# Optimization experiments

Hardware: AMD Instinct MI355X
Metric: run time of the kernel (lower is better)

Reference implementation:

```python
import jax, jax.numpy as jnp
import numpy as np

NUM_HEADS = 12
EMB = 768
D_KEY = 64
D_VALUE = 64
MASKED = True


def setup_inputs() -> dict:
    key = jax.random.key(0)
    k1, k2, k3, k4 = jax.random.split(key, 4)
    x = jax.random.normal(k1, (1, 4096, EMB), dtype=jnp.float32)
    q_proj = jax.random.normal(k2, (NUM_HEADS, EMB, D_KEY), dtype=jnp.float32)
    k_proj = jax.random.normal(k3, (NUM_HEADS, EMB, D_KEY), dtype=jnp.float32)
    v_proj = jax.random.normal(k4, (NUM_HEADS, EMB, D_VALUE), dtype=jnp.float32)
    return {"x": x, "q_proj": q_proj, "k_proj": k_proj, "v_proj": v_proj}


def reference(x, q_proj, k_proj, v_proj):
    # x: [B, S, E]; projections: [H, E, dk/dv]
    q = jnp.einsum("bse,hek->bhsk", x, q_proj)  # [B,H,S,dk]
    k = jnp.einsum("bse,hek->bhsk", x, k_proj)  # [B,H,S,dk]
    v = jnp.einsum("bse,hev->bhsv", x, v_proj)  # [B,H,S,dv]
    scale = jnp.sqrt(jnp.asarray(D_KEY, dtype=x.dtype))
    scores = jnp.einsum("bhsk,bhtk->bhst", q, k) / scale  # [B,H,S,S]
    if MASKED:
        S = x.shape[1]
        # causal mask: disallow attending to future positions (strict upper triangle)
        mask = jnp.triu(jnp.ones((S, S), dtype=bool), k=1)
        scores = jnp.where(mask, -jnp.inf, scores)
    attn = jax.nn.softmax(scores, axis=-1)
    out = jnp.einsum("bhst,bhtv->bhsv", attn, v)  # [B,H,S,dv]
    return out
```

## Files before the change

### kernel.cpp

```cpp
#include <hip/hip_runtime.h>
#include <hip/hip_bf16.h>

#define NH 12
#define SEQ 4096
#define E 768
#define DK 64

typedef float f32x4 __attribute__((ext_vector_type(4)));
typedef float f32x16 __attribute__((ext_vector_type(16)));
typedef __bf16 bf16x8 __attribute__((ext_vector_type(8)));
typedef __bf16 bf16x4 __attribute__((ext_vector_type(4)));
typedef unsigned u32x2 __attribute__((ext_vector_type(2)));
typedef unsigned u32x4 __attribute__((ext_vector_type(4)));

#define MFMA16(a, b, c) __builtin_amdgcn_mfma_f32_16x16x32_bf16((a), (b), (c), 0, 0, 0)
#define MFMA32(a, b, c) __builtin_amdgcn_mfma_f32_32x32x16_bf16((a), (b), (c), 0, 0, 0)

#define SCL 0.18033688011112042f
#define DEFER 10.8f

#define PART_SZ 4352

__device__ __forceinline__ void gload16(const void* g, void* l) {
    __builtin_amdgcn_global_load_lds(
        (const __attribute__((address_space(1))) void*)g,
        (__attribute__((address_space(3))) void*)l, 16, 0, 0);
}

__device__ __forceinline__ void block_sync() {
    __builtin_amdgcn_sched_barrier(0);
    __builtin_amdgcn_s_barrier();
    __builtin_amdgcn_sched_barrier(0);
}

__device__ __forceinline__ unsigned cvtpk(float lo, float hi) {
    unsigned r;
    asm("v_cvt_pk_bf16_f32 %0, %1, %2" : "=v"(r) : "v"(lo), "v"(hi));
    return r;
}
__device__ __forceinline__ u32x2 plswap(unsigned a, unsigned b) {
    return __builtin_amdgcn_permlane32_swap(a, b, false, false);
}
__device__ __forceinline__ float xhalf_max(float v) {
    u32x2 r = plswap(__float_as_uint(v), __float_as_uint(v));
    return fmaxf(__uint_as_float(r.x), __uint_as_float(r.y));
}
__device__ __forceinline__ float xhalf_add(float v) {
    u32x2 r = plswap(__float_as_uint(v), __float_as_uint(v));
    return __uint_as_float(r.x) + __uint_as_float(r.y);
}

__global__ __launch_bounds__(256) void prep_kernel(
    const float* __restrict__ x,
    const float* __restrict__ qp, const float* __restrict__ kp,
    const float* __restrict__ vp,
    __bf16* __restrict__ xh, __bf16* __restrict__ xl,
    __bf16* __restrict__ wtq_h, __bf16* __restrict__ wtq_l,
    __bf16* __restrict__ wtk_h, __bf16* __restrict__ wtk_l,
    __bf16* __restrict__ wtv_h) {
    __shared__ float tl[64][65];

    if (blockIdx.x >= 144) {
        int i = (blockIdx.x - 144) * 256 + threadIdx.x;
        float4 v = ((const float4*)x)[i];
        bf16x4 h, l;
        float vv[4] = {v.x, v.y, v.z, v.w};
#pragma unroll
        for (int j = 0; j < 4; ++j) {
            __bf16 hh = (__bf16)vv[j];
            h[j] = hh;
            l[j] = (__bf16)(vv[j] - (float)hh);
        }
        ((bf16x4*)xh)[i] = h;
        ((bf16x4*)xl)[i] = l;
        return;
    }

    const int h = blockIdx.x / 12;
    const int kt = blockIdx.x % 12;
    const int c = threadIdx.x & 63;
    const int r4 = threadIdx.x >> 6;

#pragma unroll
    for (int mat = 0; mat < 3; ++mat) {
        const float* src = ((mat == 0) ? qp : (mat == 1) ? kp : vp)
                         + (size_t)h * E * DK + (size_t)kt * 64 * DK;
        __syncthreads();
#pragma unroll
        for (int i = 0; i < 16; ++i) {
            int row = i * 4 + r4;
            tl[row][c] = src[row * DK + c];
        }
        __syncthreads();
#pragma unroll
        for (int i = 0; i < 16; ++i) {
            int n = i * 4 + r4;
            float v = tl[c][n];
            size_t o = (size_t)h * DK * E + (size_t)n * E + kt * 64 + c;
            if (mat == 0) {
                __bf16 hh = (__bf16)v;
                wtq_h[o] = hh;
                wtq_l[o] = (__bf16)(v - (float)hh);
            } else if (mat == 1) {
                float kk = v * SCL;
                __bf16 hh = (__bf16)kk;
                wtk_h[o] = hh;
                wtk_l[o] = (__bf16)(kk - (float)hh);
            } else {
                wtv_h[o] = (__bf16)v;
            }
        }
    }
}

__global__ __launch_bounds__(128, 2) void proj_kernel(
    const __bf16* __restrict__ xh, const __bf16* __restrict__ xl,
    const __bf16* __restrict__ wq_h_g, const __bf16* __restrict__ wq_l_g,
    const __bf16* __restrict__ wk_h_g, const __bf16* __restrict__ wk_l_g,
    const __bf16* __restrict__ wv_g,
    __bf16* __restrict__ qh_o, __bf16* __restrict__ ql_o,
    __bf16* __restrict__ kh_o, __bf16* __restrict__ kl_o,
    __bf16* __restrict__ vt_o) {
    __shared__ char wlds[2][20480];

    const int wg = (blockIdx.x & 7) * 96 + (blockIdx.x >> 3);
    const int head = wg >> 6;
    const int rb = wg & 63;
    const int wave = threadIdx.x >> 6;
    const int lane = threadIdx.x & 63;
    const int lrow = lane & 15;
    const int lk8 = (lane >> 4) * 8;
    const int g4 = (lane >> 4) * 4;
    const int rowbase = rb * 64 + wave * 32;

    const char* bases[5] = {
        (const char*)(wq_h_g + head * DK * E), (const char*)(wq_l_g + head * DK * E),
        (const char*)(wk_h_g + head * DK * E), (const char*)(wk_l_g + head * DK * E),
        (const char*)(wv_g + head * DK * E)};
    const int srow = lane >> 2;
    const int scol = (lane & 3) * 16;

    auto STAGE = [&](int buf, int ks) {
#pragma unroll
        for (int r = 0; r < 10; ++r) {
            int q = wave * 10 + r;
            const char* src = bases[q >> 2] + (size_t)((q & 3) * 16 + srow) * (E * 2) + ks * 64 + scol;
            gload16(src, wlds[buf] + q * 1024 + lane * 16);
        }
    };

    f32x4 accq[2][4], acck[2][4], accv[2][4];
#pragma unroll
    for (int rt = 0; rt < 2; ++rt)
#pragma unroll
        for (int f = 0; f < 4; ++f) {
            accq[rt][f] = (f32x4){0.f, 0.f, 0.f, 0.f};
            acck[rt][f] = (f32x4){0.f, 0.f, 0.f, 0.f};
            accv[rt][f] = (f32x4){0.f, 0.f, 0.f, 0.f};
        }

    bf16x8 ah[2], al[2], ahn[2], aln[2];
    auto LOADA = [&](int ks, bf16x8* h, bf16x8* l) {
#pragma unroll
        for (int rt = 0; rt < 2; ++rt) {
            size_t xo = (size_t)(rowbase + rt * 16 + lrow) * E + ks * 32 + lk8;
            h[rt] = *(const bf16x8*)(xh + xo);
            l[rt] = *(const bf16x8*)(xl + xo);
        }
    };

    LOADA(0, ah, al);
    STAGE(0, 0);
    int buf = 0;
    for (int ks = 0; ks < 24; ++ks) {
        if (ks < 23) {
            LOADA(ks + 1, ahn, aln);
            STAGE(buf ^ 1, ks + 1);
            asm volatile("s_waitcnt vmcnt(14)" ::: "memory");
        } else {
            asm volatile("s_waitcnt vmcnt(0)" ::: "memory");
        }
        block_sync();
#pragma unroll
        for (int f = 0; f < 4; ++f) {
            int bo = (f * 16 + lrow) * 64 + lk8 * 2;
            bf16x8 bqh = *(const bf16x8*)(wlds[buf] + bo);
            bf16x8 bql = *(const bf16x8*)(wlds[buf] + 4096 + bo);
            bf16x8 bkh = *(const bf16x8*)(wlds[buf] + 8192 + bo);
            bf16x8 bkl = *(const bf16x8*)(wlds[buf] + 12288 + bo);
            bf16x8 bv  = *(const bf16x8*)(wlds[buf] + 16384 + bo);
#pragma unroll
            for (int rt = 0; rt < 2; ++rt) {
                accq[rt][f] = MFMA16(ah[rt], bqh, accq[rt][f]);
                accq[rt][f] = MFMA16(ah[rt], bql, accq[rt][f]);
                accq[rt][f] = MFMA16(al[rt], bqh, accq[rt][f]);
                acck[rt][f] = MFMA16(ah[rt], bkh, acck[rt][f]);
                acck[rt][f] = MFMA16(ah[rt], bkl, acck[rt][f]);
                acck[rt][f] = MFMA16(al[rt], bkh, acck[rt][f]);
                accv[rt][f] = MFMA16(bv, ah[rt], accv[rt][f]);
            }
        }
        block_sync();
        if (ks < 23) {
#pragma unroll
            for (int rt = 0; rt < 2; ++rt) {
                ah[rt] = ahn[rt];
                al[rt] = aln[rt];
            }
        }
        buf ^= 1;
    }

    char* khb = (char*)kh_o + (size_t)head * SEQ * DK * 2;
    char* klb = (char*)kl_o + (size_t)head * SEQ * DK * 2;
    char* vb = (char*)vt_o + (size_t)head * DK * SEQ * 2;
#pragma unroll
    for (int rt = 0; rt < 2; ++rt)
#pragma unroll
        for (int f = 0; f < 4; ++f)
#pragma unroll
            for (int r = 0; r < 4; ++r) {
                int srow_o = rowbase + rt * 16 + g4 + r;
                int d = f * 16 + lrow;
                size_t o = (size_t)head * SEQ * DK + (size_t)srow_o * DK + d;
                float qv = accq[rt][f][r];
                __bf16 qhh = (__bf16)qv;
                qh_o[o] = qhh;
                ql_o[o] = (__bf16)(qv - (float)qhh);
                size_t ko = (size_t)(srow_o >> 6) * 8192 + ((srow_o >> 5) & 1) * 4096
                          + (size_t)f * 1024
                          + ((srow_o & 31) + 32 * ((lrow >> 3) & 1)) * 16 + (lrow & 7) * 2;
                float kv = acck[rt][f][r];
                __bf16 khh = (__bf16)kv;
                *(__bf16*)(khb + ko) = khh;
                *(__bf16*)(klb + ko) = (__bf16)(kv - (float)khh);
                int vd = f * 16 + g4 + r;
                int vs = rowbase + rt * 16 + lrow;
                size_t vo = (size_t)(vs >> 6) * 8192 + ((vd >> 5) & 1) * 4096
                          + ((vs >> 4) & 3) * 1024
                          + ((vd & 31) + 32 * ((vs >> 3) & 1)) * 16 + (vs & 7) * 2;
                *(__bf16*)(vb + vo) = (__bf16)accv[rt][f][r];
            }
}

__global__ __launch_bounds__(256, 2) void attn_part_kernel(
    const __bf16* __restrict__ qh, const __bf16* __restrict__ ql,
    const __bf16* __restrict__ kh, const __bf16* __restrict__ kl,
    const __bf16* __restrict__ vt,
    char* __restrict__ part) {
    const int blk = (blockIdx.x & 7) * 216 + (blockIdx.x >> 3);
    const int wave = threadIdx.x >> 6;
    const int task = blk * 4 + wave;
    const int lane = threadIdx.x & 63;
    const int lq = lane & 31;
    const int lh = lane >> 5;

    const int head = task / 576;
    const int t = task - head * 576;
    int g = 0;
#pragma unroll 8
    for (int gg = 1; gg <= 7; ++gg)
        if (t >= 16 * gg * (gg + 1) / 2) g = gg;
    const int nsp = g + 1;
    const int u = t - 16 * g * (g + 1) / 2;
    const int w = 16 * g + u / nsp;
    const int split = u - (u / nsp) * nsp;
    const int ktot = (w >> 1) + 1;
    const int lo = (split * ktot) / nsp;
    const int hi = ((split + 1) * ktot) / nsp;
    const int rowbase = w * 32;

    const size_t hoff = (size_t)head * SEQ * DK;

    bf16x8 qBh[4], qBl[4];
    {
        const __bf16* qph = qh + hoff + (size_t)(rowbase + lq) * DK + lh * 8;
        const __bf16* qpl = ql + hoff + (size_t)(rowbase + lq) * DK + lh * 8;
#pragma unroll
        for (int ds = 0; ds < 4; ++ds) {
            qBh[ds] = *(const bf16x8*)(qph + ds * 16);
            qBl[ds] = *(const bf16x8*)(qpl + ds * 16);
        }
    }

    const char* kh_p = (const char*)(kh + hoff) + (size_t)lo * 8192 + lane * 16;
    const char* kl_p = (const char*)(kl + hoff) + (size_t)lo * 8192 + lane * 16;
    const char* vt_p = (const char*)(vt + (size_t)head * DK * SEQ) + (size_t)lo * 8192 + lane * 16;

    f32x16 O0 = (f32x16)0.0f, O1 = (f32x16)0.0f;
    float m = -3.0e38f, lsum = 0.f;

    for (int tt = lo; tt < hi; ++tt) {
        const int kb = tt * 64;

        f32x16 s0 = (f32x16)0.0f, s1 = (f32x16)0.0f;
#pragma unroll
        for (int ds = 0; ds < 4; ++ds) {
            bf16x8 ah0 = *(const bf16x8*)(kh_p + ds * 1024);
            bf16x8 al0 = *(const bf16x8*)(kl_p + ds * 1024);
            bf16x8 ah1 = *(const bf16x8*)(kh_p + 4096 + ds * 1024);
            bf16x8 al1 = *(const bf16x8*)(kl_p + 4096 + ds * 1024);
            s0 = MFMA32(ah0, qBh[ds], s0);
            s1 = MFMA32(ah1, qBh[ds], s1);
            s0 = MFMA32(al0, qBh[ds], s0);
            s1 = MFMA32(al1, qBh[ds], s1);
            s0 = MFMA32(ah0, qBl[ds], s0);
            s1 = MFMA32(ah1, qBl[ds], s1);
        }

        bf16x8 v00 = *(const bf16x8*)(vt_p + 0);
        bf16x8 v01 = *(const bf16x8*)(vt_p + 1024);
        bf16x8 v10 = *(const bf16x8*)(vt_p + 2048);
        bf16x8 v11 = *(const bf16x8*)(vt_p + 3072);
        bf16x8 w00 = *(const bf16x8*)(vt_p + 4096);
        bf16x8 w01 = *(const bf16x8*)(vt_p + 5120);
        bf16x8 w10 = *(const bf16x8*)(vt_p + 6144);
        bf16x8 w11 = *(const bf16x8*)(vt_p + 7168);

        if (kb + 63 > rowbase) {
            int qa = rowbase + lq;
#pragma unroll
            for (int r = 0; r < 16; ++r) {
                int kp = kb + ((r & 3) + 8 * (r >> 2) + 4 * lh);
                if (kp > qa) s0[r] = -1.0e30f;
                if (kp + 32 > qa) s1[r] = -1.0e30f;
            }
        }

        float x0 = fmaxf(s0[0], s0[1]), x1 = fmaxf(s0[2], s0[3]);
        float x2 = fmaxf(s0[4], s0[5]), x3 = fmaxf(s0[6], s0[7]);
#pragma unroll
        for (int r = 8; r < 16; r += 4) {
            x0 = fmaxf(x0, fmaxf(s0[r], s0[r + 1]));
            x1 = fmaxf(x1, fmaxf(s0[r + 2], s0[r + 3]));
        }
#pragma unroll
        for (int r = 0; r < 16; r += 4) {
            x2 = fmaxf(x2, fmaxf(s1[r], s1[r + 1]));
            x3 = fmaxf(x3, fmaxf(s1[r + 2], s1[r + 3]));
        }
        float mx = xhalf_max(fmaxf(fmaxf(x0, x1), fmaxf(x2, x3)));

        if (!__all(mx - m <= DEFER)) {
            float mn = fmaxf(m, mx);
            float al = exp2f(m - mn);
            m = mn;
            lsum *= al;
#pragma unroll
            for (int r = 0; r < 16; ++r) {
                float a = __shfl(al, (r & 3) + 8 * (r >> 2) + 4 * lh);
                O0[r] *= a;
                O1[r] *= a;
            }
        }

        s0 = s0 - m;
        s1 = s1 - m;
#pragma unroll
        for (int r = 0; r < 16; ++r) {
            s0[r] = exp2f(s0[r]);
            s1[r] = exp2f(s1[r]);
        }
        {
            f32x16 sv = s0 + s1;
            float p0 = 0.f, p1 = 0.f;
#pragma unroll
            for (int r = 0; r < 16; r += 4) {
                p0 += sv[r] + sv[r + 1];
                p1 += sv[r + 2] + sv[r + 3];
            }
            lsum += p0 + p1;
        }

        unsigned W0 = cvtpk(s0[0], s0[1]), W1 = cvtpk(s0[2], s0[3]);
        unsigned W2 = cvtpk(s0[4], s0[5]), W3 = cvtpk(s0[6], s0[7]);
        unsigned W4 = cvtpk(s0[8], s0[9]), W5 = cvtpk(s0[10], s0[11]);
        unsigned W6 = cvtpk(s0[12], s0[13]), W7 = cvtpk(s0[14], s0[15]);
        u32x2 rA = plswap(W0, W2), rB = plswap(W1, W3);
        u32x2 rC = plswap(W4, W6), rD = plswap(W5, W7);
        bf16x8 p00 = __builtin_bit_cast(bf16x8, (u32x4){rA.x, rB.x, rA.y, rB.y});
        bf16x8 p01 = __builtin_bit_cast(bf16x8, (u32x4){rC.x, rD.x, rC.y, rD.y});
        W0 = cvtpk(s1[0], s1[1]); W1 = cvtpk(s1[2], s1[3]);
        W2 = cvtpk(s1[4], s1[5]); W3 = cvtpk(s1[6], s1[7]);
        W4 = cvtpk(s1[8], s1[9]); W5 = cvtpk(s1[10], s1[11]);
        W6 = cvtpk(s1[12], s1[13]); W7 = cvtpk(s1[14], s1[15]);
        rA = plswap(W0, W2); rB = plswap(W1, W3);
        rC = plswap(W4, W6); rD = plswap(W5, W7);
        bf16x8 p10 = __builtin_bit_cast(bf16x8, (u32x4){rA.x, rB.x, rA.y, rB.y});
        bf16x8 p11 = __builtin_bit_cast(bf16x8, (u32x4){rC.x, rD.x, rC.y, rD.y});

        O0 = MFMA32(p00, v00, O0);
        O0 = MFMA32(p01, v01, O0);
        O0 = MFMA32(p10, v10, O0);
        O0 = MFMA32(p11, v11, O0);
        O1 = MFMA32(p00, w00, O1);
        O1 = MFMA32(p01, w01, O1);
        O1 = MFMA32(p10, w10, O1);
        O1 = MFMA32(p11, w11, O1);

        kh_p += 8192;
        kl_p += 8192;
        vt_p += 8192;
    }

    char* pb = part + (size_t)task * PART_SZ;
    unsigned* ph = (unsigned*)pb;
#pragma unroll
    for (int r = 0; r < 16; r += 2) {
        ph[(r >> 1) * 64 + lane] = cvtpk(O0[r], O0[r + 1]);
        ph[512 + (r >> 1) * 64 + lane] = cvtpk(O1[r], O1[r + 1]);
    }
    float lf = xhalf_add(lsum);
    float* pm = (float*)(pb + 4096);
    if (lane < 32) {
        pm[lq] = m;
        pm[32 + lq] = lf;
    }
}

__global__ __launch_bounds__(256) void attn_comb_kernel(
    const char* __restrict__ part, float* __restrict__ out) {
    const int W = blockIdx.x;
    const int head = W >> 7, w = W & 127;
    const int g = w >> 4;
    const int nsp = g + 1;
    const int tb = head * 576 + 16 * g * (g + 1) / 2 + (w - 16 * g) * nsp;

    const int tid = threadIdx.x;
    const int row = tid >> 3;
    const int d0 = (tid & 7) * 8;
    const int lane0 = (d0 & 31) + 32 * ((row >> 2) & 1);
    const int r = (row & 3) + 4 * (row >> 3);
    const int word = (r >> 1) * 64;
    const int hi16 = r & 1;
    const char* p0 = part + (size_t)tb * PART_SZ;

    float mstar = -3.0e38f;
    for (int s = 0; s < nsp; ++s) {
        const float* pm = (const float*)(p0 + s * PART_SZ + 4096);
        mstar = fmaxf(mstar, pm[row]);
    }

    float acc[8] = {0.f, 0.f, 0.f, 0.f, 0.f, 0.f, 0.f, 0.f};
    float lt = 0.f;
    for (int s = 0; s < nsp; ++s) {
        const char* ps = p0 + s * PART_SZ;
        const float* pm = (const float*)(ps + 4096);
        float wgt = exp2f(pm[row] - mstar);
        lt += wgt * pm[32 + row];
        const unsigned* pw = (const unsigned*)(ps + (d0 >> 5) * 2048);
        u32x4 a = *(const u32x4*)(pw + word + lane0);
        u32x4 b = *(const u32x4*)(pw + word + lane0 + 4);
#pragma unroll
        for (int j = 0; j < 8; ++j) {
            unsigned u = (j < 4) ? a[j] : b[j - 4];
            unsigned bits = hi16 ? (u & 0xffff0000u) : (u << 16);
            acc[j] += wgt * __uint_as_float(bits);
        }
    }
    float inv = 1.0f / lt;
    size_t o = (size_t)head * SEQ * DK + (size_t)(w * 32 + row) * DK + d0;
#pragma unroll
    for (int j = 0; j < 8; ++j) out[o + j] = acc[j] * inv;
}

extern "C" void kernel_launch(void* const* d_in, const int* in_sizes, int n_in,
                              void* d_out, int out_size, void* d_ws, size_t ws_size,
                              hipStream_t stream) {
    const float* x = (const float*)d_in[0];
    const float* qp = (const float*)d_in[1];
    const float* kp = (const float*)d_in[2];
    const float* vp = (const float*)d_in[3];
    float* out = (float*)d_out;

    const size_t WT_SZ = (size_t)NH * DK * E * 2;
    const size_t QKV_SZ = (size_t)NH * SEQ * DK * 2;
    const size_t X_SZ = (size_t)SEQ * E * 2;
    char* ws = (char*)d_ws;
    __bf16* wtq_h = (__bf16*)(ws + 0 * WT_SZ);
    __bf16* wtq_l = (__bf16*)(ws + 1 * WT_SZ);
    __bf16* wtk_h = (__bf16*)(ws + 2 * WT_SZ);
    __bf16* wtk_l = (__bf16*)(ws + 3 * WT_SZ);
    __bf16* wtv_h = (__bf16*)(ws + 4 * WT_SZ);
    char* px = ws + 5 * WT_SZ;
    __bf16* xh = (__bf16*)(px + 0 * X_SZ);
    __bf16* xl = (__bf16*)(px + 1 * X_SZ);
    char* p2 = px + 2 * X_SZ;
    __bf16* qh = (__bf16*)(p2 + 0 * QKV_SZ);
    __bf16* ql = (__bf16*)(p2 + 1 * QKV_SZ);
    __bf16* kh = (__bf16*)(p2 + 2 * QKV_SZ);
    __bf16* kl = (__bf16*)(p2 + 3 * QKV_SZ);
    __bf16* vt = (__bf16*)(p2 + 4 * QKV_SZ);
    char* part = p2 + 5 * QKV_SZ;

    hipLaunchKernelGGL(prep_kernel, dim3(144 + SEQ * E / 4 / 256), dim3(256), 0, stream,
                       x, qp, kp, vp, xh, xl, wtq_h, wtq_l, wtk_h, wtk_l, wtv_h);
    hipLaunchKernelGGL(proj_kernel, dim3(768), dim3(128), 0, stream,
                       xh, xl, wtq_h, wtq_l, wtk_h, wtk_l, wtv_h, qh, ql, kh, kl, vt);
    hipLaunchKernelGGL(attn_part_kernel, dim3(1728), dim3(256), 0, stream,
                       qh, ql, kh, kl, vt, part);
    hipLaunchKernelGGL(attn_comb_kernel, dim3(1536), dim3(256), 0, stream,
                       part, out);
}
```

Before: 151.7 us.

## Split projection work across four waves by output column slice

The projection kernel moves from 2 waves per block, each covering 32 rows and all 64 output columns, to 4 waves each covering all 64 rows and one 16-column slice. Each wave now loads all of the block's x rows (four row tiles) but only one B fragment per matrix, and weight staging is spread over four waves. This doubles the waves available to hide latency and shrinks per-wave accumulator state. In exchange, every wave redundantly loads the full x tile from global memory, so x traffic per block rises fourfold.

```diff
diff --git a/kernel.cpp b/kernel.cpp
--- a/kernel.cpp
+++ b/kernel.cpp
@@ -113,7 +113,7 @@
     }
 }
 
-__global__ __launch_bounds__(128, 2) void proj_kernel(
+__global__ __launch_bounds__(256, 2) void proj_kernel(
     const __bf16* __restrict__ xh, const __bf16* __restrict__ xl,
     const __bf16* __restrict__ wq_h_g, const __bf16* __restrict__ wq_l_g,
     const __bf16* __restrict__ wk_h_g, const __bf16* __restrict__ wk_l_g,
@@ -131,7 +131,7 @@
     const int lrow = lane & 15;
     const int lk8 = (lane >> 4) * 8;
     const int g4 = (lane >> 4) * 4;
-    const int rowbase = rb * 64 + wave * 32;
+    const int rowbase = rb * 64;
 
     const char* bases[5] = {
         (const char*)(wq_h_g + head * DK * E), (const char*)(wq_l_g + head * DK * E),
@@ -142,27 +142,25 @@
 
     auto STAGE = [&](int buf, int ks) {
 #pragma unroll
-        for (int r = 0; r < 10; ++r) {
-            int q = wave * 10 + r;
+        for (int r = 0; r < 5; ++r) {
+            int q = wave * 5 + r;
             const char* src = bases[q >> 2] + (size_t)((q & 3) * 16 + srow) * (E * 2) + ks * 64 + scol;
             gload16(src, wlds[buf] + q * 1024 + lane * 16);
         }
     };
 
-    f32x4 accq[2][4], acck[2][4], accv[2][4];
-#pragma unroll
-    for (int rt = 0; rt < 2; ++rt)
-#pragma unroll
-        for (int f = 0; f < 4; ++f) {
-            accq[rt][f] = (f32x4){0.f, 0.f, 0.f, 0.f};
-            acck[rt][f] = (f32x4){0.f, 0.f, 0.f, 0.f};
-            accv[rt][f] = (f32x4){0.f, 0.f, 0.f, 0.f};
-        }
-
-    bf16x8 ah[2], al[2], ahn[2], aln[2];
+    f32x4 accq[4], acck[4], accv[4];
+#pragma unroll
+    for (int rt = 0; rt < 4; ++rt) {
+        accq[rt] = (f32x4){0.f, 0.f, 0.f, 0.f};
+        acck[rt] = (f32x4){0.f, 0.f, 0.f, 0.f};
+        accv[rt] = (f32x4){0.f, 0.f, 0.f, 0.f};
+    }
+
+    bf16x8 ah[4], al[4], ahn[4], aln[4];
     auto LOADA = [&](int ks, bf16x8* h, bf16x8* l) {
 #pragma unroll
-        for (int rt = 0; rt < 2; ++rt) {
+        for (int rt = 0; rt < 4; ++rt) {
             size_t xo = (size_t)(rowbase + rt * 16 + lrow) * E + ks * 32 + lk8;
             h[rt] = *(const bf16x8*)(xh + xo);
             l[rt] = *(const bf16x8*)(xl + xo);
@@ -176,34 +174,33 @@
         if (ks < 23) {
             LOADA(ks + 1, ahn, aln);
             STAGE(buf ^ 1, ks + 1);
-            asm volatile("s_waitcnt vmcnt(14)" ::: "memory");
+            asm volatile("s_waitcnt vmcnt(13)" ::: "memory");
         } else {
             asm volatile("s_waitcnt vmcnt(0)" ::: "memory");
         }
         block_sync();
-#pragma unroll
-        for (int f = 0; f < 4; ++f) {
-            int bo = (f * 16 + lrow) * 64 + lk8 * 2;
+        {
+            int bo = (wave * 16 + lrow) * 64 + lk8 * 2;
             bf16x8 bqh = *(const bf16x8*)(wlds[buf] + bo);
             bf16x8 bql = *(const bf16x8*)(wlds[buf] + 4096 + bo);
             bf16x8 bkh = *(const bf16x8*)(wlds[buf] + 8192 + bo);
             bf16x8 bkl = *(const bf16x8*)(wlds[buf] + 12288 + bo);
             bf16x8 bv  = *(const bf16x8*)(wlds[buf] + 16384 + bo);
 #pragma unroll
-            for (int rt = 0; rt < 2; ++rt) {
-                accq[rt][f] = MFMA16(ah[rt], bqh, accq[rt][f]);
-                accq[rt][f] = MFMA16(ah[rt], bql, accq[rt][f]);
-                accq[rt][f] = MFMA16(al[rt], bqh, accq[rt][f]);
-                acck[rt][f] = MFMA16(ah[rt], bkh, acck[rt][f]);
-                acck[rt][f] = MFMA16(ah[rt], bkl, acck[rt][f]);
-                acck[rt][f] = MFMA16(al[rt], bkh, acck[rt][f]);
-                accv[rt][f] = MFMA16(bv, ah[rt], accv[rt][f]);
+            for (int rt = 0; rt < 4; ++rt) {
+                accq[rt] = MFMA16(ah[rt], bqh, accq[rt]);
+                accq[rt] = MFMA16(ah[rt], bql, accq[rt]);
+                accq[rt] = MFMA16(al[rt], bqh, accq[rt]);
+                acck[rt] = MFMA16(ah[rt], bkh, acck[rt]);
+                acck[rt] = MFMA16(ah[rt], bkl, acck[rt]);
+                acck[rt] = MFMA16(al[rt], bkh, acck[rt]);
+                accv[rt] = MFMA16(bv, ah[rt], accv[rt]);
             }
         }
         block_sync();
         if (ks < 23) {
 #pragma unroll
-            for (int rt = 0; rt < 2; ++rt) {
+            for (int rt = 0; rt < 4; ++rt) {
                 ah[rt] = ahn[rt];
                 al[rt] = aln[rt];
             }
@@ -215,32 +212,30 @@
     char* klb = (char*)kl_o + (size_t)head * SEQ * DK * 2;
     char* vb = (char*)vt_o + (size_t)head * DK * SEQ * 2;
 #pragma unroll
-    for (int rt = 0; rt < 2; ++rt)
-#pragma unroll
-        for (int f = 0; f < 4; ++f)
-#pragma unroll
-            for (int r = 0; r < 4; ++r) {
-                int srow_o = rowbase + rt * 16 + g4 + r;
-                int d = f * 16 + lrow;
-                size_t o = (size_t)head * SEQ * DK + (size_t)srow_o * DK + d;
-                float qv = accq[rt][f][r];
-                __bf16 qhh = (__bf16)qv;
-                qh_o[o] = qhh;
-                ql_o[o] = (__bf16)(qv - (float)qhh);
-                size_t ko = (size_t)(srow_o >> 6) * 8192 + ((srow_o >> 5) & 1) * 4096
-                          + (size_t)f * 1024
-                          + ((srow_o & 31) + 32 * ((lrow >> 3) & 1)) * 16 + (lrow & 7) * 2;
-                float kv = acck[rt][f][r];
-                __bf16 khh = (__bf16)kv;
-                *(__bf16*)(khb + ko) = khh;
-                *(__bf16*)(klb + ko) = (__bf16)(kv - (float)khh);
-                int vd = f * 16 + g4 + r;
-                int vs = rowbase + rt * 16 + lrow;
-                size_t vo = (size_t)(vs >> 6) * 8192 + ((vd >> 5) & 1) * 4096
-                          + ((vs >> 4) & 3) * 1024
-                          + ((vd & 31) + 32 * ((vs >> 3) & 1)) * 16 + (vs & 7) * 2;
-                *(__bf16*)(vb + vo) = (__bf16)accv[rt][f][r];
-            }
+    for (int rt = 0; rt < 4; ++rt)
+#pragma unroll
+        for (int r = 0; r < 4; ++r) {
+            int srow_o = rowbase + rt * 16 + g4 + r;
+            int d = wave * 16 + lrow;
+            size_t o = (size_t)head * SEQ * DK + (size_t)srow_o * DK + d;
+            float qv = accq[rt][r];
+            __bf16 qhh = (__bf16)qv;
+            qh_o[o] = qhh;
+            ql_o[o] = (__bf16)(qv - (float)qhh);
+            size_t ko = (size_t)(srow_o >> 6) * 8192 + ((srow_o >> 5) & 1) * 4096
+                      + (size_t)wave * 1024
+                      + ((srow_o & 31) + 32 * ((lrow >> 3) & 1)) * 16 + (lrow & 7) * 2;
+            float kv = acck[rt][r];
+            __bf16 khh = (__bf16)kv;
+            *(__bf16*)(khb + ko) = khh;
+            *(__bf16*)(klb + ko) = (__bf16)(kv - (float)khh);
+            int vd = wave * 16 + g4 + r;
+            int vs = rowbase + rt * 16 + lrow;
+            size_t vo = (size_t)(vs >> 6) * 8192 + ((vd >> 5) & 1) * 4096
+                      + ((vs >> 4) & 3) * 1024
+                      + ((vd & 31) + 32 * ((vs >> 3) & 1)) * 16 + (vs & 7) * 2;
+            *(__bf16*)(vb + vo) = (__bf16)accv[rt][r];
+        }
 }
 
 __global__ __launch_bounds__(256, 2) void attn_part_kernel(
@@ -495,7 +490,7 @@
 
     hipLaunchKernelGGL(prep_kernel, dim3(144 + SEQ * E / 4 / 256), dim3(256), 0, stream,
                        x, qp, kp, vp, xh, xl, wtq_h, wtq_l, wtk_h, wtk_l, wtv_h);
-    hipLaunchKernelGGL(proj_kernel, dim3(768), dim3(128), 0, stream,
+    hipLaunchKernelGGL(proj_kernel, dim3(768), dim3(256), 0, stream,
                        xh, xl, wtq_h, wtq_l, wtk_h, wtk_l, wtv_h, qh, ql, kh, kl, vt);
     hipLaunchKernelGGL(attn_part_kernel, dim3(1728), dim3(256), 0, stream,
                        qh, ql, kh, kl, vt, part);
```

Result: slower. 188.1 us (+24.0%).
